# Kernel optimization log

Measured on AMD Instinct MI355X. Metric: run time of the kernel, lower is better.

Reference implementation:

```python
import jax, jax.numpy as jnp
import numpy as np

B, M, D, DE = 2, 256, 256, 64  # batch, tokens, in_dim, dep_embed_dim


def setup_inputs() -> dict:
    key = jax.random.key(0)
    ks = jax.random.split(key, 10)
    features = jax.random.normal(ks[0], (B, M + 1, D), jnp.float32)
    dep_type_adj = jax.random.normal(ks[1], (B, M, M, DE), jnp.float32)
    adj = (jax.random.uniform(ks[2], (B, M, M)) < 0.05).astype(jnp.int32)
    idx = jnp.arange(M)
    adj = adj.at[:, idx, idx].set(1)
    asp_start = jax.random.randint(ks[3], (B,), 0, 200, dtype=jnp.int32)
    asp_end = asp_start + 16
    s = lambda fan_in: 1.0 / np.sqrt(fan_in)
    Wz = jax.random.normal(ks[4], (D, D), jnp.float32) * s(D)
    bz = jax.random.normal(ks[5], (D,), jnp.float32) * s(D)
    Wa = jax.random.normal(ks[6], (D + DE + D,), jnp.float32) * s(D + DE + D)
    Wm = jax.random.normal(ks[7], (D, D + DE), jnp.float32) * s(D + DE)
    Wh = jax.random.normal(ks[8], (D, 2 * D), jnp.float32) * s(2 * D)
    return dict(features=features, dep_type_adj=dep_type_adj, deprel_adj=adj,
                asp_start=asp_start, asp_end=asp_end,
                Wz=Wz, bz=bz, Wa=Wa, Wm=Wm, Wh=Wh)


def reference(features, dep_type_adj, deprel_adj, asp_start, asp_end, Wz, bz, Wa, Wm, Wh):
    # z_linear
    zf = features @ Wz.T + bz                              # [B, M+1, D]
    f = zf[:, 1:]                                          # token feats [B, M, D]
    asp = zf[0, 1:]                                        # NOTE: original indexes features[0] (batch 0)

    # candidate neighbors for node i: out-edges (i,j) then in-edges (j,i) -> 2M slots
    dep_cat = jnp.concatenate([dep_type_adj, jnp.swapaxes(dep_type_adj, 1, 2)], axis=2)  # [B,M,2M,DE]
    mask = jnp.concatenate([deprel_adj, jnp.swapaxes(deprel_adj, 1, 2)], axis=2) != 0    # [B,M,2M]

    # attention_layer weight split over [dep | neighbor_feat | aspect_feat]
    wa_dep, wa_nf, wa_asp = Wa[:DE], Wa[DE:DE + D], Wa[DE + D:]
    s = (jnp.einsum('bike,e->bik', dep_cat, wa_dep)
         + jnp.tile(f @ wa_nf, (1, 2))[:, None, :]
         + (asp @ wa_asp)[None, :, None])                  # [B,M,2M]
    s = jnp.where(s > 0, s, 0.01 * s)                      # LeakyReLU(0.01)
    big_neg = jnp.finfo(s.dtype).min
    w = jax.nn.softmax(jnp.where(mask, s, big_neg), axis=-1)
    w = jnp.where(mask, w, 0.0)                            # edge-softmax over valid neighbors

    # w_m over [dep | neighbor_feat]
    Wm_dep, Wm_f = Wm[:, :DE], Wm[:, DE:]
    nf_proj = jnp.tile(f @ Wm_f.T, (1, 2, 1))              # [B,2M,D], neighbor part (i-independent)
    msg = jax.nn.relu(jnp.einsum('bike,de->bikd', dep_cat, Wm_dep) + nf_proj[:, None])  # [B,M,2M,D]
    fused = jnp.einsum('bik,bikd->bid', w, msg)            # weighted aggregate [B,M,D]

    # w_h over [fused | aspect]
    out_asp = jax.nn.relu(fused @ Wh[:, :D].T + (asp @ Wh[:, D:].T)[None])  # [B,M,D]

    # only aspect-span nodes are updated; +1 offset into the token axis
    pos = jnp.arange(M)
    upd = (pos[None, :] >= asp_start[:, None]) & (pos[None, :] < asp_end[:, None])  # [B,M]
    tokens = jnp.where(upd[..., None], out_asp, features[:, 1:])
    return jnp.concatenate([features[:, :1], tokens], axis=1)  # dropout is identity at inference
```

## Files before the change

kernel.cpp:

```cpp
#include <hip/hip_runtime.h>
#include <hip/hip_bf16.h>
#include <cstdint>

#define BB 2
#define MM 256
#define DD 256
#define DE 64
#define K2 (2*MM)
#define WM_LD (DD+DE)
#define WH_LD (2*DD)

__device__ float g_fz   [MM*DD];
__device__ float g_fproj[BB*MM*DD];
__device__ float g_fnf  [BB*MM];
__device__ float g_WzT  [DD*DD];
__device__ float g_WmT  [DD*DD];

__global__ __launch_bounds__(256) void k_tr(const float* __restrict__ Wz,
                                            const float* __restrict__ Wm,
                                            const float4* __restrict__ src,
                                            float4* __restrict__ dst, int n4) {
  const int t = threadIdx.x;
  const int blk = blockIdx.x;
  const int d = blk & 255;
  if (blk < 256) g_WzT[t*DD + d] = Wz[(size_t)d*DD + t];
  else           g_WmT[t*DD + d] = Wm[(size_t)d*WM_LD + DE + t];
  const int idx = blk*256 + t;
  if (idx < n4) dst[idx] = src[idx];
}

__global__ __launch_bounds__(256) void k_pre(const float* __restrict__ feats,
                                             const float* __restrict__ bz,
                                             const float* __restrict__ Wa) {
  const int blk = blockIdx.x;
  const int b   = blk >> 7;
  const int m0  = (blk & 127) * 2;
  const int t   = threadIdx.x;

  __shared__ float fin[2][DD];
  __shared__ float fzsh[2][DD];

  fin[0][t] = feats[((size_t)b*(MM+1) + m0 + 1)*DD + t];
  fin[1][t] = feats[((size_t)b*(MM+1) + m0 + 2)*DD + t];
  __syncthreads();

  float a0 = 0.f, a1 = 0.f;
  #pragma unroll 8
  for (int e4 = 0; e4 < DD/4; ++e4) {
    const float4 f0 = *(const float4*)&fin[0][e4*4];
    const float4 f1 = *(const float4*)&fin[1][e4*4];
    const float w0 = g_WzT[(e4*4+0)*DD + t];
    const float w1 = g_WzT[(e4*4+1)*DD + t];
    const float w2 = g_WzT[(e4*4+2)*DD + t];
    const float w3 = g_WzT[(e4*4+3)*DD + t];
    a0 += f0.x*w0 + f0.y*w1 + f0.z*w2 + f0.w*w3;
    a1 += f1.x*w0 + f1.y*w1 + f1.z*w2 + f1.w*w3;
  }
  const float bzt = bz[t];
  a0 += bzt; a1 += bzt;
  fzsh[0][t] = a0; fzsh[1][t] = a1;
  if (b == 0) {
    g_fz[(size_t)(m0    )*DD + t] = a0;
    g_fz[(size_t)(m0 + 1)*DD + t] = a1;
  }
  __syncthreads();

  const int wv = t >> 6, lane = t & 63;
  if (wv < 2) {
    float p = 0.f;
    for (int e = lane; e < DD; e += 64) p += fzsh[wv][e] * Wa[DE + e];
    for (int off = 32; off > 0; off >>= 1) p += __shfl_down(p, off, 64);
    if (lane == 0) g_fnf[b*MM + m0 + wv] = p;
  }

  float p0 = 0.f, p1 = 0.f;
  #pragma unroll 8
  for (int e4 = 0; e4 < DD/4; ++e4) {
    const float4 f0 = *(const float4*)&fzsh[0][e4*4];
    const float4 f1 = *(const float4*)&fzsh[1][e4*4];
    const float w0 = g_WmT[(e4*4+0)*DD + t];
    const float w1 = g_WmT[(e4*4+1)*DD + t];
    const float w2 = g_WmT[(e4*4+2)*DD + t];
    const float w3 = g_WmT[(e4*4+3)*DD + t];
    p0 += f0.x*w0 + f0.y*w1 + f0.z*w2 + f0.w*w3;
    p1 += f1.x*w0 + f1.y*w1 + f1.z*w2 + f1.w*w3;
  }
  g_fproj[((size_t)b*MM + m0    )*DD + t] = p0;
  g_fproj[((size_t)b*MM + m0 + 1)*DD + t] = p1;
}

__global__ __launch_bounds__(256) void k_attn(const float* __restrict__ dta,
                                              const int*   __restrict__ adj,
                                              const int*   __restrict__ a_start,
                                              const int*   __restrict__ a_end,
                                              const float* __restrict__ Wa,
                                              const float* __restrict__ Wm,
                                              const float* __restrict__ Wh,
                                              float* __restrict__ out) {
  const int b = blockIdx.x >> 4;
  const int r = blockIdx.x & 15;
  const int i = a_start[b] + r;
  if (i >= a_end[b] || i >= MM) return;
  const int t = threadIdx.x;

  __shared__ int   act[K2];
  __shared__ float sv [K2];
  __shared__ float red[256];
  __shared__ int   wcnt[4];
  __shared__ float wadep[DE];
  __shared__ float fz0[DD];
  __shared__ float depsh[64*DE];
  __shared__ float fused_sh[DD];
  __shared__ float aspd_sh;

  if (t < DE) wadep[t] = Wa[t];
  fz0[t] = g_fz[(size_t)i*DD + t];
  __syncthreads();

  red[t] = fz0[t] * Wa[DE + DD + t];
  __syncthreads();
  for (int s = 128; s > 0; s >>= 1) { if (t < s) red[t] += red[t+s]; __syncthreads(); }
  if (t == 0) aspd_sh = red[0];
  __syncthreads();
  const float aspdot_i = aspd_sh;

  const int lane = t & 63, wv = t >> 6;
  int na = 0;
  for (int phase = 0; phase < 2; ++phase) {
    const int k = phase*256 + t;
    const int mval = (k < MM) ? adj[((size_t)b*MM + i)*MM + k]
                              : adj[((size_t)b*MM + (k - MM))*MM + i];
    const bool on = (mval != 0);
    const unsigned long long bal = __ballot(on);
    if (lane == 0) wcnt[wv] = __popcll(bal);
    __syncthreads();
    int off = na;
    for (int w2 = 0; w2 < wv; ++w2) off += wcnt[w2];
    off += __popcll(bal & ((1ull << lane) - 1ull));
    if (on) act[off] = k;
    na += wcnt[0] + wcnt[1] + wcnt[2] + wcnt[3];
    __syncthreads();
  }

  for (int j = t; j < na; j += 256) {
    const int k = act[j];
    const float* dv = (k < MM) ? dta + (((size_t)b*MM + i)*MM + k)*DE
                               : dta + (((size_t)b*MM + (k - MM))*MM + i)*DE;
    float s = 0.f;
    const float4* dv4 = (const float4*)dv;
    #pragma unroll
    for (int e4 = 0; e4 < DE/4; ++e4) {
      const float4 v = dv4[e4];
      s += v.x*wadep[4*e4] + v.y*wadep[4*e4+1] + v.z*wadep[4*e4+2] + v.w*wadep[4*e4+3];
    }
    s += g_fnf[b*MM + (k & (MM-1))] + aspdot_i;
    sv[j] = (s > 0.f) ? s : 0.01f * s;
  }
  __syncthreads();

  float part = -3.4e38f;
  for (int j = t; j < na; j += 256) part = fmaxf(part, sv[j]);
  red[t] = part; __syncthreads();
  for (int s = 128; s > 0; s >>= 1) { if (t < s) red[t] = fmaxf(red[t], red[t+s]); __syncthreads(); }
  const float mx = red[0];
  __syncthreads();
  float psum = 0.f;
  for (int j = t; j < na; j += 256) { float e = expf(sv[j] - mx); sv[j] = e; psum += e; }
  red[t] = psum; __syncthreads();
  for (int s = 128; s > 0; s >>= 1) { if (t < s) red[t] += red[t+s]; __syncthreads(); }
  const float inv = 1.f / red[0];
  __syncthreads();
  for (int j = t; j < na; j += 256) sv[j] *= inv;
  __syncthreads();

  const int d = t;
  float wm[DE];
  {
    const float4* wmrow = (const float4*)(Wm + (size_t)d * WM_LD);
    #pragma unroll
    for (int e4 = 0; e4 < DE/4; ++e4) {
      float4 v = wmrow[e4];
      wm[4*e4] = v.x; wm[4*e4+1] = v.y; wm[4*e4+2] = v.z; wm[4*e4+3] = v.w;
    }
  }
  float acc = 0.f;
  for (int base = 0; base < na; base += 64) {
    const int cnt = min(64, na - base);
    const int nf4 = cnt * (DE/4);
    for (int q = t; q < nf4; q += 256) {
      const int jl = q >> 4, e4 = q & 15;
      const int k = act[base + jl];
      const float* dv = (k < MM) ? dta + (((size_t)b*MM + i)*MM + k)*DE
                                 : dta + (((size_t)b*MM + (k - MM))*MM + i)*DE;
      ((float4*)(depsh + jl*DE))[e4] = ((const float4*)dv)[e4];
    }
    __syncthreads();
    for (int jl = 0; jl < cnt; ++jl) {
      const float* dp = depsh + jl*DE;
      float dot = 0.f;
      #pragma unroll
      for (int e4 = 0; e4 < DE/4; ++e4) {
        const float4 v = *(const float4*)(dp + 4*e4);
        dot += v.x*wm[4*e4] + v.y*wm[4*e4+1] + v.z*wm[4*e4+2] + v.w*wm[4*e4+3];
      }
      const int k = act[base + jl];
      float msg = dot + g_fproj[((size_t)b*MM + (k & (MM-1)))*DD + d];
      msg = (msg > 0.f) ? msg : 0.f;
      acc += sv[base + jl] * msg;
    }
    __syncthreads();
  }
  fused_sh[d] = acc;
  __syncthreads();

  const float4* whrow = (const float4*)(Wh + (size_t)d * WH_LD);
  float o = 0.f;
  #pragma unroll 4
  for (int e4 = 0; e4 < DD/4; ++e4) {
    const float4 v = whrow[e4];
    const float* fp = &fused_sh[e4*4];
    o += v.x*fp[0] + v.y*fp[1] + v.z*fp[2] + v.w*fp[3];
  }
  #pragma unroll 4
  for (int e4 = 0; e4 < DD/4; ++e4) {
    const float4 v = whrow[DD/4 + e4];
    const float* fp = &fz0[e4*4];
    o += v.x*fp[0] + v.y*fp[1] + v.z*fp[2] + v.w*fp[3];
  }
  out[((size_t)b*(MM+1) + i + 1)*DD + d] = (o > 0.f) ? o : 0.f;
}

extern "C" void kernel_launch(void* const* d_in, const int* in_sizes, int n_in,
                              void* d_out, int out_size, void* d_ws, size_t ws_size,
                              hipStream_t stream) {
  const float* feats   = (const float*)d_in[0];
  const float* dta     = (const float*)d_in[1];
  const int*   adj     = (const int*)  d_in[2];
  const int*   a_start = (const int*)  d_in[3];
  const int*   a_end   = (const int*)  d_in[4];
  const float* Wz      = (const float*)d_in[5];
  const float* bz      = (const float*)d_in[6];
  const float* Wa      = (const float*)d_in[7];
  const float* Wm      = (const float*)d_in[8];
  const float* Wh      = (const float*)d_in[9];
  float* out = (float*)d_out;

  const int n4 = BB*(MM+1)*DD/4;
  k_tr  <<<2*DD, 256, 0, stream>>>(Wz, Wm, (const float4*)feats, (float4*)out, n4);
  k_pre <<<BB*MM/2, 256, 0, stream>>>(feats, bz, Wa);
  k_attn<<<BB*16, 256, 0, stream>>>(dta, adj, a_start, a_end, Wa, Wm, Wh, out);
}
```

Measured before the change: 148.3 us.

## Pre-transpose Wm dep and Wh weights, use wave shuffles for reductions

```diff
diff --git a/kernel.cpp b/kernel.cpp
--- a/kernel.cpp
+++ b/kernel.cpp
@@ -10,23 +10,35 @@
 #define WM_LD (DD+DE)
 #define WH_LD (2*DD)
 
-__device__ float g_fz   [MM*DD];
-__device__ float g_fproj[BB*MM*DD];
-__device__ float g_fnf  [BB*MM];
-__device__ float g_WzT  [DD*DD];
-__device__ float g_WmT  [DD*DD];
+__device__ float g_fz    [MM*DD];
+__device__ float g_fproj [BB*MM*DD];
+__device__ float g_fnf   [BB*MM];
+__device__ float g_WzT   [DD*DD];
+__device__ float g_WmT   [DD*DD];
+__device__ float g_WmDepT[DE*DD];
+__device__ float g_WhT   [2*DD*DD];
 
 __global__ __launch_bounds__(256) void k_tr(const float* __restrict__ Wz,
                                             const float* __restrict__ Wm,
+                                            const float* __restrict__ Wh,
                                             const float4* __restrict__ src,
                                             float4* __restrict__ dst, int n4) {
   const int t = threadIdx.x;
   const int blk = blockIdx.x;
-  const int d = blk & 255;
-  if (blk < 256) g_WzT[t*DD + d] = Wz[(size_t)d*DD + t];
-  else           g_WmT[t*DD + d] = Wm[(size_t)d*WM_LD + DE + t];
-  const int idx = blk*256 + t;
-  if (idx < n4) dst[idx] = src[idx];
+  if (blk < 256) {
+    const int d = blk;
+    g_WzT[t*DD + d] = Wz[(size_t)d*DD + t];
+  } else if (blk < 512) {
+    const int d = blk - 256;
+    g_WmT[t*DD + d] = Wm[(size_t)d*WM_LD + DE + t];
+    if (t < DE) g_WmDepT[t*DD + d] = Wm[(size_t)d*WM_LD + t];
+  } else {
+    const int idx = blk - 512;
+    const int d = idx & 255, half = idx >> 8;
+    g_WhT[(size_t)(half*DD + t)*DD + d] = Wh[(size_t)d*WH_LD + half*DD + t];
+  }
+  const int gidx = blk*256 + t;
+  if (gidx < n4) dst[gidx] = src[gidx];
 }
 
 __global__ __launch_bounds__(256) void k_pre(const float* __restrict__ feats,
@@ -94,53 +106,55 @@
                                               const int*   __restrict__ a_start,
                                               const int*   __restrict__ a_end,
                                               const float* __restrict__ Wa,
-                                              const float* __restrict__ Wm,
-                                              const float* __restrict__ Wh,
                                               float* __restrict__ out) {
   const int b = blockIdx.x >> 4;
   const int r = blockIdx.x & 15;
   const int i = a_start[b] + r;
   if (i >= a_end[b] || i >= MM) return;
   const int t = threadIdx.x;
+  const int lane = t & 63, wv = t >> 6;
 
   __shared__ int   act[K2];
   __shared__ float sv [K2];
-  __shared__ float red[256];
-  __shared__ int   wcnt[4];
+  __shared__ int   wcnt[8];
+  __shared__ float wr  [4];
+  __shared__ float wrm [4];
+  __shared__ float wrs [4];
   __shared__ float wadep[DE];
   __shared__ float fz0[DD];
   __shared__ float depsh[64*DE];
   __shared__ float fused_sh[DD];
-  __shared__ float aspd_sh;
-
+
+  const int mval0 = adj[((size_t)b*MM + i)*MM + t];
+  const int mval1 = adj[((size_t)b*MM + t)*MM + i];
+  const float myfz = g_fz[(size_t)i*DD + t];
+  fz0[t] = myfz;
   if (t < DE) wadep[t] = Wa[t];
-  fz0[t] = g_fz[(size_t)i*DD + t];
-  __syncthreads();
-
-  red[t] = fz0[t] * Wa[DE + DD + t];
-  __syncthreads();
-  for (int s = 128; s > 0; s >>= 1) { if (t < s) red[t] += red[t+s]; __syncthreads(); }
-  if (t == 0) aspd_sh = red[0];
-  __syncthreads();
-  const float aspdot_i = aspd_sh;
-
-  const int lane = t & 63, wv = t >> 6;
-  int na = 0;
-  for (int phase = 0; phase < 2; ++phase) {
-    const int k = phase*256 + t;
-    const int mval = (k < MM) ? adj[((size_t)b*MM + i)*MM + k]
-                              : adj[((size_t)b*MM + (k - MM))*MM + i];
-    const bool on = (mval != 0);
-    const unsigned long long bal = __ballot(on);
-    if (lane == 0) wcnt[wv] = __popcll(bal);
-    __syncthreads();
-    int off = na;
-    for (int w2 = 0; w2 < wv; ++w2) off += wcnt[w2];
-    off += __popcll(bal & ((1ull << lane) - 1ull));
-    if (on) act[off] = k;
-    na += wcnt[0] + wcnt[1] + wcnt[2] + wcnt[3];
-    __syncthreads();
-  }
+
+  {
+    float p = myfz * Wa[DE + DD + t];
+    for (int off = 32; off > 0; off >>= 1) p += __shfl_down(p, off, 64);
+    if (lane == 0) wr[wv] = p;
+  }
+
+  const bool on0 = (mval0 != 0);
+  const bool on1 = (mval1 != 0);
+  const unsigned long long b0 = __ballot(on0);
+  const unsigned long long b1 = __ballot(on1);
+  if (lane == 0) { wcnt[wv] = __popcll(b0); wcnt[4+wv] = __popcll(b1); }
+  __syncthreads();
+  const float aspdot_i = wr[0] + wr[1] + wr[2] + wr[3];
+  const int tot0 = wcnt[0] + wcnt[1] + wcnt[2] + wcnt[3];
+  const int na   = tot0 + wcnt[4] + wcnt[5] + wcnt[6] + wcnt[7];
+  {
+    int off0 = 0, off1 = tot0;
+    for (int w2 = 0; w2 < wv; ++w2) { off0 += wcnt[w2]; off1 += wcnt[4+w2]; }
+    off0 += __popcll(b0 & ((1ull << lane) - 1ull));
+    off1 += __popcll(b1 & ((1ull << lane) - 1ull));
+    if (on0) act[off0] = t;
+    if (on1) act[off1] = MM + t;
+  }
+  __syncthreads();
 
   for (int j = t; j < na; j += 256) {
     const int k = act[j];
@@ -156,33 +170,27 @@
     s += g_fnf[b*MM + (k & (MM-1))] + aspdot_i;
     sv[j] = (s > 0.f) ? s : 0.01f * s;
   }
-  __syncthreads();
-
-  float part = -3.4e38f;
-  for (int j = t; j < na; j += 256) part = fmaxf(part, sv[j]);
-  red[t] = part; __syncthreads();
-  for (int s = 128; s > 0; s >>= 1) { if (t < s) red[t] = fmaxf(red[t], red[t+s]); __syncthreads(); }
-  const float mx = red[0];
-  __syncthreads();
-  float psum = 0.f;
-  for (int j = t; j < na; j += 256) { float e = expf(sv[j] - mx); sv[j] = e; psum += e; }
-  red[t] = psum; __syncthreads();
-  for (int s = 128; s > 0; s >>= 1) { if (t < s) red[t] += red[t+s]; __syncthreads(); }
-  const float inv = 1.f / red[0];
-  __syncthreads();
-  for (int j = t; j < na; j += 256) sv[j] *= inv;
-  __syncthreads();
+  {
+    float part = -3.4e38f;
+    for (int j = t; j < na; j += 256) part = fmaxf(part, sv[j]);
+    for (int off = 32; off > 0; off >>= 1) part = fmaxf(part, __shfl_down(part, off, 64));
+    if (lane == 0) wrm[wv] = part;
+  }
+  __syncthreads();
+  const float mx = fmaxf(fmaxf(wrm[0], wrm[1]), fmaxf(wrm[2], wrm[3]));
+  {
+    float psum = 0.f;
+    for (int j = t; j < na; j += 256) { float e = expf(sv[j] - mx); sv[j] = e; psum += e; }
+    for (int off = 32; off > 0; off >>= 1) psum += __shfl_down(psum, off, 64);
+    if (lane == 0) wrs[wv] = psum;
+  }
+  __syncthreads();
+  const float inv = 1.f / (wrs[0] + wrs[1] + wrs[2] + wrs[3]);
 
   const int d = t;
   float wm[DE];
-  {
-    const float4* wmrow = (const float4*)(Wm + (size_t)d * WM_LD);
-    #pragma unroll
-    for (int e4 = 0; e4 < DE/4; ++e4) {
-      float4 v = wmrow[e4];
-      wm[4*e4] = v.x; wm[4*e4+1] = v.y; wm[4*e4+2] = v.z; wm[4*e4+3] = v.w;
-    }
-  }
+  #pragma unroll 8
+  for (int e = 0; e < DE; ++e) wm[e] = g_WmDepT[e*DD + d];
   float acc = 0.f;
   for (int base = 0; base < na; base += 64) {
     const int cnt = min(64, na - base);
@@ -210,23 +218,14 @@
     }
     __syncthreads();
   }
-  fused_sh[d] = acc;
-  __syncthreads();
-
-  const float4* whrow = (const float4*)(Wh + (size_t)d * WH_LD);
+  fused_sh[d] = acc * inv;
+  __syncthreads();
+
   float o = 0.f;
-  #pragma unroll 4
-  for (int e4 = 0; e4 < DD/4; ++e4) {
-    const float4 v = whrow[e4];
-    const float* fp = &fused_sh[e4*4];
-    o += v.x*fp[0] + v.y*fp[1] + v.z*fp[2] + v.w*fp[3];
-  }
-  #pragma unroll 4
-  for (int e4 = 0; e4 < DD/4; ++e4) {
-    const float4 v = whrow[DD/4 + e4];
-    const float* fp = &fz0[e4*4];
-    o += v.x*fp[0] + v.y*fp[1] + v.z*fp[2] + v.w*fp[3];
-  }
+  #pragma unroll 8
+  for (int e = 0; e < DD; ++e) o += fused_sh[e] * g_WhT[(size_t)e*DD + d];
+  #pragma unroll 8
+  for (int e = 0; e < DD; ++e) o += fz0[e] * g_WhT[(size_t)(DD + e)*DD + d];
   out[((size_t)b*(MM+1) + i + 1)*DD + d] = (o > 0.f) ? o : 0.f;
 }
 
@@ -246,7 +245,7 @@
   float* out = (float*)d_out;
 
   const int n4 = BB*(MM+1)*DD/4;
-  k_tr  <<<2*DD, 256, 0, stream>>>(Wz, Wm, (const float4*)feats, (float4*)out, n4);
+  k_tr  <<<1024, 256, 0, stream>>>(Wz, Wm, Wh, (const float4*)feats, (float4*)out, n4);
   k_pre <<<BB*MM/2, 256, 0, stream>>>(feats, bz, Wa);
-  k_attn<<<BB*16, 256, 0, stream>>>(dta, adj, a_start, a_end, Wa, Wm, Wh, out);
-}
+  k_attn<<<BB*16, 256, 0, stream>>>(dta, adj, a_start, a_end, Wa, out);
+}
```

Measured after the change: 155.3 us. 1.05x slower.
